# Kernel tuning notes

Hardware: AMD Instinct MI355X
Metric: run time of the kernel (lower is better)

The kernel has to match this reference:

```python
import jax, jax.numpy as jnp
import numpy as np

RADIUS = 3
LEVELS = (1, 4)
P = 3


def _corr_level(fm, gm, cds, jj, radius):
    """Radius-windowed bilinear gather-correlation at one pyramid level.
    fm:  [N, C, Hl, Wl]  feature maps at this level
    gm:  [E, C, P, P]    gathered source patch features (gmap[ii])
    cds: [E, P, P, 2]    (x, y) sampling coords in this level's pixel units
    jj:  [E]             target frame index per edge
    returns [E, 2r+1, 2r+1, P, P]
    """
    N, C, Hl, Wl = fm.shape
    E, _, Pp, _ = gm.shape
    fm_flat = jnp.transpose(fm, (0, 2, 3, 1)).reshape(N * Hl * Wl, C)  # [NHW, C]
    x = cds[..., 0]
    y = cds[..., 1]
    x0 = jnp.floor(x)
    y0 = jnp.floor(y)
    fx = x - x0  # bilinear fractions
    fy = y - y0
    x0i = x0.astype(jnp.int32)
    y0i = y0.astype(jnp.int32)
    D = 2 * radius + 2  # integer support window covering all 2r+1 shifted bilinear taps
    offs = jnp.arange(D, dtype=jnp.int32) - radius
    gy = jnp.clip(y0i[..., None] + offs, 0, Hl - 1)  # [E,P,P,D]
    gx = jnp.clip(x0i[..., None] + offs, 0, Wl - 1)  # [E,P,P,D]
    base = (jj.astype(jnp.int32) * (Hl * Wl))[:, None, None, None, None]  # [E,1,1,1,1]
    lin = base + gy[..., :, None] * Wl + gx[..., None, :]  # [E,P,P,D,D]
    lin_per = jnp.moveaxis(lin.reshape(E, Pp, Pp, D * D), -1, 0)  # [D*D,E,P,P]
    gmT = jnp.transpose(gm, (0, 2, 3, 1))  # [E,P,P,C]

    def step(carry, idx):
        vals = jnp.take(fm_flat, idx, axis=0)  # [E,P,P,C] gathered features
        return carry, jnp.sum(vals * gmT, axis=-1)  # channel contraction -> [E,P,P]

    _, cw = jax.lax.scan(jax.checkpoint(step), None, lin_per)  # [D*D,E,P,P]
    cw = jnp.moveaxis(cw, 0, -1).reshape(E, Pp, Pp, D, D)
    w00 = ((1 - fy) * (1 - fx))[..., None, None]
    w01 = ((1 - fy) * fx)[..., None, None]
    w10 = (fy * (1 - fx))[..., None, None]
    w11 = (fy * fx)[..., None, None]
    c = (w00 * cw[..., : D - 1, : D - 1]
         + w01 * cw[..., : D - 1, 1:]
         + w10 * cw[..., 1:, : D - 1]
         + w11 * cw[..., 1:, 1:])  # [E,P,P,2r+1,2r+1]
    return jnp.transpose(c, (0, 3, 4, 1, 2))  # [E,2r+1,2r+1,P,P]


def _forward(fmap, gmap, coords, ii, jj):
    fm0 = fmap[0]  # [N,C,H,W] level 1
    N, C, H, W = fm0.shape
    # pyramidify: level-4 map via 4x4 average pooling
    fm1 = fm0.reshape(N, C, H // 4, 4, W // 4, 4).mean(axis=(3, 5))
    gm = gmap[0][ii]  # [E,C,P,P]
    cds = coords[0]  # [E,P,P,2]
    c0 = _corr_level(fm0, gm, cds / LEVELS[0], jj, RADIUS)
    c1 = _corr_level(fm1, gm, cds / LEVELS[1], jj, RADIUS)
    out = jnp.stack([c0, c1], axis=-1)  # [E,7,7,P,P,2]
    return out.reshape(1, cds.shape[0], -1)  # [1,E,2*49*P*P]


def setup_inputs():
    key = jax.random.key(0)
    k = jax.random.split(key, 5)
    N, C, H, W = 16, 128, 120, 160
    M = 16 * 96  # frames * patches_per_image
    E = 8192  # edges in the patch graph
    fmap = jax.random.normal(k[0], (1, N, C, H, W), jnp.float32)
    gmap = jax.random.normal(k[1], (1, M, C, P, P), jnp.float32)
    # patch centers kept in-bounds for both pyramid levels
    u = jax.random.uniform(k[2], (1, E, 1, 1, 2), jnp.float32)
    lo = jnp.array([13.0, 13.0], jnp.float32)
    span = jnp.array([126.0, 86.0], jnp.float32)  # x in [13,139], y in [13,99]
    dy, dx = jnp.meshgrid(jnp.arange(P) - 1, jnp.arange(P) - 1, indexing='ij')
    patch_offs = jnp.stack([dx, dy], axis=-1).astype(jnp.float32)  # [P,P,2] (x,y)
    coords = lo + u * span + patch_offs  # [1,E,P,P,2]
    ii = jax.random.randint(k[3], (E,), 0, M, dtype=jnp.int32)
    jj = jax.random.randint(k[4], (E,), 0, N, dtype=jnp.int32)
    return {"fmap": fmap, "gmap": gmap, "coords": coords, "ii": ii, "jj": jj}


def reference(fmap, gmap, coords, ii, jj):
    return _forward(fmap, gmap, coords, ii, jj)
```

## Files before the change

kernel.cpp:

```cpp
#include <hip/hip_runtime.h>

#define RADIUS 3
#define C_CH 128
#define NG 16
#define N_FR 16
#define H0 120
#define W0 160
#define HW0 (H0*W0)
#define H1 30
#define W1 40
#define HW1 (H1*W1)
#define EXT 10
#define NCELL 100
#define M_PT 1536
#define FM1SZ (N_FR*H1*W1*C_CH)
#define GT_SZ (M_PT*9*C_CH)
#define SCSTR 12
#define NBKT 256

typedef _Float16 half2v __attribute__((ext_vector_type(2)));
union Q { uint4 u4; half2v h[4]; };

#if __has_builtin(__builtin_amdgcn_fdot2)
#define FDOT2(a,b,c) __builtin_amdgcn_fdot2((a),(b),(c),false)
#else
#define FDOT2(a,b,c) ((c) + (float)(a).x*(float)(b).x + (float)(a).y*(float)(b).y)
#endif

__device__ __forceinline__ unsigned pack2h(float a, float b) {
    union { _Float16 h[2]; unsigned u; } x;
    x.h[0] = (_Float16)a; x.h[1] = (_Float16)b;
    return x.u;
}

__global__ __launch_bounds__(256) void pack_fmap2(const float* __restrict__ fm0,
                                                  uint4* __restrict__ fH) {
    int idx = blockIdx.x * 256 + threadIdx.x;
    int total = N_FR * NG * HW0;
    if (idx >= total) return;
    int xy = idx % HW0;
    int g = (idx / HW0) & (NG - 1);
    int n = idx / (HW0 * NG);
    const float* src = fm0 + ((size_t)(n * C_CH + g * 8)) * HW0 + xy;
    uint4 o;
    o.x = pack2h(src[0],          src[(size_t)HW0]);
    o.y = pack2h(src[2*(size_t)HW0], src[3*(size_t)HW0]);
    o.z = pack2h(src[4*(size_t)HW0], src[5*(size_t)HW0]);
    o.w = pack2h(src[6*(size_t)HW0], src[7*(size_t)HW0]);
    fH[idx] = o;
}

__global__ __launch_bounds__(256) void pool_from_fH(const uint4* __restrict__ fH,
                                                    uint4* __restrict__ f1H) {
    int idx = blockIdx.x * 256 + threadIdx.x;
    int total = N_FR * NG * HW1;
    if (idx >= total) return;
    int xo = idx % W1;
    int yo = (idx / W1) % H1;
    int ng = idx / HW1;
    const uint4* src = fH + ((size_t)ng * H0 + yo * 4) * W0 + xo * 4;
    float s[8];
#pragma unroll
    for (int k = 0; k < 8; ++k) s[k] = 0.f;
#pragma unroll
    for (int yl = 0; yl < 4; ++yl) {
#pragma unroll
        for (int dx = 0; dx < 4; ++dx) {
            Q q; q.u4 = src[(size_t)yl * W0 + dx];
#pragma unroll
            for (int k = 0; k < 4; ++k) {
                s[2*k]   += (float)q.h[k].x;
                s[2*k+1] += (float)q.h[k].y;
            }
        }
    }
    uint4 o;
    o.x = pack2h(s[0] * (1.f/16.f), s[1] * (1.f/16.f));
    o.y = pack2h(s[2] * (1.f/16.f), s[3] * (1.f/16.f));
    o.z = pack2h(s[4] * (1.f/16.f), s[5] * (1.f/16.f));
    o.w = pack2h(s[6] * (1.f/16.f), s[7] * (1.f/16.f));
    f1H[idx] = o;
}

__global__ __launch_bounds__(128) void gpack(const float* __restrict__ g,
                                             unsigned* __restrict__ gH) {
    __shared__ float s[C_CH * 9];
    int m = blockIdx.x;
    const float* src = g + (size_t)m * (C_CH * 9);
    for (int t = threadIdx.x; t < C_CH * 9; t += 128) s[t] = src[t];
    __syncthreads();
    unsigned* dst = gH + (size_t)m * (9 * 64);
    for (int t = threadIdx.x; t < 9 * 64; t += 128) {
        int pq = t >> 6, pr = t & 63;
        dst[t] = pack2h(s[(2 * pr) * 9 + pq], s[(2 * pr + 1) * 9 + pq]);
    }
}

__device__ __forceinline__ int sort_key(const int* jj, const float* coords, int e) {
    float cy = coords[(size_t)e * 18 + 1];
    int by0 = (int)floorf(cy) - RADIUS;
    int band = min(max(by0 >> 3, 0), 15);
    return jj[e] * 16 + band;
}

__global__ void zero_kernel(int* cnt) {
    int t = blockIdx.x * blockDim.x + threadIdx.x;
    if (t < 2 * NBKT) cnt[t] = 0;
}

__global__ void hist_kernel(const int* __restrict__ jj, const float* __restrict__ coords,
                            int* __restrict__ cnt, int E) {
    __shared__ int h[NBKT];
    int tid = threadIdx.x;
    h[tid] = 0;
    __syncthreads();
    int e = blockIdx.x * blockDim.x + tid;
    if (e < E) atomicAdd(&h[sort_key(jj, coords, e)], 1);
    __syncthreads();
    if (h[tid] > 0) atomicAdd(&cnt[tid], h[tid]);
}

__global__ void scan_kernel(const int* __restrict__ cnt, int* __restrict__ off) {
    if (threadIdx.x == 0) {
        int s = 0;
        for (int f = 0; f < NBKT; ++f) { off[f] = s; s += cnt[f]; }
    }
}

__global__ void scatter_kernel(const int* __restrict__ jj, const float* __restrict__ coords,
                               int* __restrict__ off, int* __restrict__ perm, int E) {
    __shared__ int h[NBKT];
    __shared__ int base[NBKT];
    int tid = threadIdx.x;
    h[tid] = 0;
    __syncthreads();
    int e = blockIdx.x * blockDim.x + tid;
    int k = 0, rank = 0;
    if (e < E) {
        k = sort_key(jj, coords, e);
        rank = atomicAdd(&h[k], 1);
    }
    __syncthreads();
    if (h[tid] > 0) base[tid] = atomicAdd(&off[tid], h[tid]);
    __syncthreads();
    if (e < E) perm[base[k] + rank] = e;
}

__global__ __launch_bounds__(128) void corr_h(
        const unsigned* __restrict__ fH,
        const unsigned* __restrict__ f1H,
        const unsigned* __restrict__ gH,
        const float* __restrict__ coords,
        const int* __restrict__ ii,
        const int* __restrict__ jj,
        const int* __restrict__ perm,
        float* __restrict__ out) {
    __shared__ float sC[2 * NCELL * SCSTR];

    int nwg = gridDim.x;
    int q = nwg >> 3, r = nwg & 7;
    int xcd = blockIdx.x & 7;
    int i = blockIdx.x >> 3;
    int orig = (xcd < r ? xcd * (q + 1) : r * (q + 1) + (xcd - r) * q) + i;
    int e = perm ? perm[orig] : orig;

    int tid = threadIdx.x;
    int iie = __builtin_amdgcn_readfirstlane(ii[e]);
    int jje = __builtin_amdgcn_readfirstlane(jj[e]);
    const float* cb = coords + (size_t)e * 18;

    float cx = cb[0], cy = cb[1];
    int bx0 = (int)floorf(cx) - RADIUS;
    int by0 = (int)floorf(cy) - RADIUS;
    int bx1 = (int)floorf(cx * 0.25f) - RADIUS;
    int by1 = (int)floorf(cy * 0.25f) - RADIUS;

    int cell = min(tid, NCELL - 1);
    int iy = cell / EXT, ix = cell - iy * EXT;
    int gy0 = min(max(by0 + iy, 0), H0 - 1);
    int gx0 = min(max(bx0 + ix, 0), W0 - 1);
    int gy1 = min(max(by1 + iy, 0), H1 - 1);
    int gx1 = min(max(bx1 + ix, 0), W1 - 1);

    const uint4* f0p = (const uint4*)fH + ((size_t)jje * NG * HW0 + (size_t)gy0 * W0 + gx0);
    const uint4* f1p = (const uint4*)f1H + ((size_t)jje * NG * HW1 + (size_t)gy1 * W1 + gx1);
    const uint4* gp  = (const uint4*)gH + (size_t)iie * 144;

    float acc0[9], acc1[9];
#pragma unroll
    for (int pq = 0; pq < 9; ++pq) { acc0[pq] = 0.f; acc1[pq] = 0.f; }

#pragma unroll 4
    for (int g = 0; g < NG; ++g) {
        Q a0; a0.u4 = f0p[(size_t)g * HW0];
        Q a1; a1.u4 = f1p[(size_t)g * HW1];
#pragma unroll
        for (int pq = 0; pq < 9; ++pq) {
            Q gg; gg.u4 = gp[pq * 16 + g];
#pragma unroll
            for (int k = 0; k < 4; ++k) {
                acc0[pq] = FDOT2(a0.h[k], gg.h[k], acc0[pq]);
                acc1[pq] = FDOT2(a1.h[k], gg.h[k], acc1[pq]);
            }
        }
    }

    if (tid < NCELL) {
        float* s0 = &sC[cell * SCSTR];
        float* s1 = &sC[NCELL * SCSTR + cell * SCSTR];
        *reinterpret_cast<float4*>(s0)     = float4{acc0[0], acc0[1], acc0[2], acc0[3]};
        *reinterpret_cast<float4*>(s0 + 4) = float4{acc0[4], acc0[5], acc0[6], acc0[7]};
        s0[8] = acc0[8];
        *reinterpret_cast<float4*>(s1)     = float4{acc1[0], acc1[1], acc1[2], acc1[3]};
        *reinterpret_cast<float4*>(s1 + 4) = float4{acc1[4], acc1[5], acc1[6], acc1[7]};
        s1[8] = acc1[8];
    }
    __syncthreads();

    for (int o = tid; o < 882; o += 128) {
        int lvl = o & 1;
        int rr = o >> 1;
        int pq = rr % 9;
        int ab = rr / 9;
        int a = ab / 7, b = ab - a * 7;
        float s = lvl ? 0.25f : 1.f;
        float x = cb[pq * 2 + 0] * s;
        float y = cb[pq * 2 + 1] * s;
        float x0f = floorf(x), y0f = floorf(y);
        float fx = x - x0f, fy = y - y0f;
        int offx = (int)x0f - RADIUS - (lvl ? bx1 : bx0);
        int offy = (int)y0f - RADIUS - (lvl ? by1 : by0);
        int cell2 = (offy + a) * EXT + (offx + b);
        int base = lvl * (NCELL * SCSTR) + cell2 * SCSTR + pq;
        float c00 = sC[base];
        float c01 = sC[base + SCSTR];
        float c10 = sC[base + EXT * SCSTR];
        float c11 = sC[base + EXT * SCSTR + SCSTR];
        float v = (1.f - fy) * (1.f - fx) * c00 + (1.f - fy) * fx * c01
                + fy * (1.f - fx) * c10 + fy * fx * c11;
        out[(size_t)e * 882 + (size_t)rr * 2 + lvl] = v;
    }
}

__global__ __launch_bounds__(256) void pool_fm1T(const float* __restrict__ fm0,
                                                 float* __restrict__ fm1T) {
    __shared__ float s[C_CH * 41];
    int blk = blockIdx.x;
    int yo = blk % H1;
    int n = blk / H1;
    for (int pair = threadIdx.x; pair < C_CH * W1; pair += 256) {
        int c = pair / W1, xo = pair - c * W1;
        const float* p = fm0 + (((size_t)(n * C_CH + c) * H0) + yo * 4) * W0 + xo * 4;
        float sum = 0.f;
#pragma unroll
        for (int yl = 0; yl < 4; ++yl) {
            float4 v = *reinterpret_cast<const float4*>(p + yl * W0);
            sum += v.x + v.y + v.z + v.w;
        }
        s[c * 41 + xo] = sum * (1.f / 16.f);
    }
    __syncthreads();
    float* dp = fm1T + (size_t)blk * W1 * C_CH;
    for (int t = threadIdx.x; t < W1 * C_CH; t += 256) {
        int xo = t >> 7, c = t & 127;
        dp[t] = s[c * 41 + xo];
    }
}

__global__ __launch_bounds__(128) void corr_kernel(
        const float* __restrict__ fmap, const float* __restrict__ fm1T,
        const float* __restrict__ gmap, const float* __restrict__ coords,
        const int* __restrict__ ii, const int* __restrict__ jj,
        float* __restrict__ out) {
    __shared__ float sC[2 * NCELL * SCSTR];
    int e = blockIdx.x;
    int tid = threadIdx.x;
    int iie = __builtin_amdgcn_readfirstlane(ii[e]);
    int jje = __builtin_amdgcn_readfirstlane(jj[e]);
    const float* cb = coords + (size_t)e * 18;
    float cx = cb[0], cy = cb[1];
    int bx0 = (int)floorf(cx) - RADIUS;
    int by0 = (int)floorf(cy) - RADIUS;
    int bx1 = (int)floorf(cx * 0.25f) - RADIUS;
    int by1 = (int)floorf(cy * 0.25f) - RADIUS;
    int cell = min(tid, NCELL - 1);
    int iy = cell / EXT, ix = cell - iy * EXT;
    int gy0 = min(max(by0 + iy, 0), H0 - 1);
    int gx0 = min(max(bx0 + ix, 0), W0 - 1);
    int gy1 = min(max(by1 + iy, 0), H1 - 1);
    int gx1 = min(max(bx1 + ix, 0), W1 - 1);
    const float* fp0 = fmap + (size_t)jje * C_CH * HW0 + gy0 * W0 + gx0;
    const float* fp1 = fm1T + (((size_t)jje * H1 + gy1) * W1 + gx1) * C_CH;
    float acc0[9], acc1[9];
#pragma unroll
    for (int pq = 0; pq < 9; ++pq) { acc0[pq] = 0.f; acc1[pq] = 0.f; }
    const float* gp = gmap + (size_t)iie * (C_CH * 9);
#pragma unroll 2
    for (int c = 0; c < C_CH; c += 4) {
        float f0 = fp0[(size_t)(c + 0) * HW0];
        float f1 = fp0[(size_t)(c + 1) * HW0];
        float f2 = fp0[(size_t)(c + 2) * HW0];
        float f3 = fp0[(size_t)(c + 3) * HW0];
        float4 fv = *reinterpret_cast<const float4*>(fp1 + c);
#pragma unroll
        for (int pq = 0; pq < 9; ++pq) {
            float g0 = gp[(c + 0) * 9 + pq];
            float g1 = gp[(c + 1) * 9 + pq];
            float g2 = gp[(c + 2) * 9 + pq];
            float g3 = gp[(c + 3) * 9 + pq];
            acc0[pq] += f0 * g0 + f1 * g1 + f2 * g2 + f3 * g3;
            acc1[pq] += fv.x * g0 + fv.y * g1 + fv.z * g2 + fv.w * g3;
        }
    }
    if (tid < NCELL) {
        float* s0 = &sC[cell * SCSTR];
        float* s1 = &sC[NCELL * SCSTR + cell * SCSTR];
        *reinterpret_cast<float4*>(s0)     = float4{acc0[0], acc0[1], acc0[2], acc0[3]};
        *reinterpret_cast<float4*>(s0 + 4) = float4{acc0[4], acc0[5], acc0[6], acc0[7]};
        s0[8] = acc0[8];
        *reinterpret_cast<float4*>(s1)     = float4{acc1[0], acc1[1], acc1[2], acc1[3]};
        *reinterpret_cast<float4*>(s1 + 4) = float4{acc1[4], acc1[5], acc1[6], acc1[7]};
        s1[8] = acc1[8];
    }
    __syncthreads();
    for (int o = tid; o < 882; o += 128) {
        int lvl = o & 1;
        int rr = o >> 1;
        int pq = rr % 9;
        int ab = rr / 9;
        int a = ab / 7, b = ab - a * 7;
        float s = lvl ? 0.25f : 1.f;
        float x = cb[pq * 2 + 0] * s;
        float y = cb[pq * 2 + 1] * s;
        float x0f = floorf(x), y0f = floorf(y);
        float fx = x - x0f, fy = y - y0f;
        int offx = (int)x0f - RADIUS - (lvl ? bx1 : bx0);
        int offy = (int)y0f - RADIUS - (lvl ? by1 : by0);
        int cell2 = (offy + a) * EXT + (offx + b);
        int base = lvl * (NCELL * SCSTR) + cell2 * SCSTR + pq;
        float c00 = sC[base];
        float c01 = sC[base + SCSTR];
        float c10 = sC[base + EXT * SCSTR];
        float c11 = sC[base + EXT * SCSTR + SCSTR];
        float v = (1.f - fy) * (1.f - fx) * c00 + (1.f - fy) * fx * c01
                + fy * (1.f - fx) * c10 + fy * fx * c11;
        out[(size_t)e * 882 + (size_t)rr * 2 + lvl] = v;
    }
}

extern "C" void kernel_launch(void* const* d_in, const int* in_sizes, int n_in,
                              void* d_out, int out_size, void* d_ws, size_t ws_size,
                              hipStream_t stream) {
    const float* fmap   = (const float*)d_in[0];
    const float* gmap   = (const float*)d_in[1];
    const float* coords = (const float*)d_in[2];
    const int* ii       = (const int*)d_in[3];
    const int* jj       = (const int*)d_in[4];
    float* out = (float*)d_out;
    int E = in_sizes[3];

    size_t szFH  = (size_t)N_FR * C_CH * HW0 * 2;
    size_t szF1H = (size_t)N_FR * C_CH * HW1 * 2;
    size_t szGH  = (size_t)M_PT * 9 * C_CH * 2;
    size_t need_h = szFH + szF1H + szGH + 2048 + (size_t)E * 4;

    if (ws_size >= need_h) {
        uint4* fH  = (uint4*)d_ws;
        uint4* f1H = (uint4*)((char*)d_ws + szFH);
        unsigned* gH = (unsigned*)((char*)d_ws + szFH + szF1H);
        int* cnt  = (int*)((char*)d_ws + szFH + szF1H + szGH);
        int* off  = cnt + NBKT;
        int* perm = off + NBKT;

        int tot_pack = N_FR * NG * HW0;
        pack_fmap2<<<(tot_pack + 255) / 256, 256, 0, stream>>>(fmap, fH);
        int tot_pool = N_FR * NG * HW1;
        pool_from_fH<<<(tot_pool + 255) / 256, 256, 0, stream>>>(fH, f1H);
        gpack<<<M_PT, 128, 0, stream>>>(gmap, gH);

        int nb = (E + NBKT - 1) / NBKT;
        zero_kernel<<<(2 * NBKT + 255) / 256, 256, 0, stream>>>(cnt);
        hist_kernel<<<nb, NBKT, 0, stream>>>(jj, coords, cnt, E);
        scan_kernel<<<1, 64, 0, stream>>>(cnt, off);
        scatter_kernel<<<nb, NBKT, 0, stream>>>(jj, coords, off, perm, E);

        corr_h<<<E, 128, 0, stream>>>((const unsigned*)fH, (const unsigned*)f1H, gH,
                                      coords, ii, jj, perm, out);
        return;
    }

    float* fm1T = (float*)d_ws;
    pool_fm1T<<<N_FR * H1, 256, 0, stream>>>(fmap, fm1T);
    corr_kernel<<<E, 128, 0, stream>>>(fmap, fm1T, gmap, coords, ii, jj, out);
}
```

Before: 123.2 us.

## Compute correlation window with MFMA 16x16x32 f16 instead of fdot2

```diff
diff --git a/kernel.cpp b/kernel.cpp
--- a/kernel.cpp
+++ b/kernel.cpp
@@ -14,18 +14,14 @@
 #define NCELL 100
 #define M_PT 1536
 #define FM1SZ (N_FR*H1*W1*C_CH)
-#define GT_SZ (M_PT*9*C_CH)
 #define SCSTR 12
 #define NBKT 256
 
 typedef _Float16 half2v __attribute__((ext_vector_type(2)));
+typedef _Float16 f16x8 __attribute__((ext_vector_type(8)));
+typedef float f32x4 __attribute__((ext_vector_type(4)));
 union Q { uint4 u4; half2v h[4]; };
-
-#if __has_builtin(__builtin_amdgcn_fdot2)
-#define FDOT2(a,b,c) __builtin_amdgcn_fdot2((a),(b),(c),false)
-#else
-#define FDOT2(a,b,c) ((c) + (float)(a).x*(float)(b).x + (float)(a).y*(float)(b).y)
-#endif
+union AB { uint4 u4; f16x8 h8; };
 
 __device__ __forceinline__ unsigned pack2h(float a, float b) {
     union { _Float16 h[2]; unsigned u; } x;
@@ -43,7 +39,7 @@
     int n = idx / (HW0 * NG);
     const float* src = fm0 + ((size_t)(n * C_CH + g * 8)) * HW0 + xy;
     uint4 o;
-    o.x = pack2h(src[0],          src[(size_t)HW0]);
+    o.x = pack2h(src[0],             src[(size_t)HW0]);
     o.y = pack2h(src[2*(size_t)HW0], src[3*(size_t)HW0]);
     o.z = pack2h(src[4*(size_t)HW0], src[5*(size_t)HW0]);
     o.w = pack2h(src[6*(size_t)HW0], src[7*(size_t)HW0]);
@@ -146,10 +142,10 @@
     if (e < E) perm[base[k] + rank] = e;
 }
 
-__global__ __launch_bounds__(128) void corr_h(
-        const unsigned* __restrict__ fH,
-        const unsigned* __restrict__ f1H,
-        const unsigned* __restrict__ gH,
+__global__ __launch_bounds__(64, 4) void corr_mfma(
+        const uint4* __restrict__ fH,
+        const uint4* __restrict__ f1H,
+        const uint4* __restrict__ gH4,
         const float* __restrict__ coords,
         const int* __restrict__ ii,
         const int* __restrict__ jj,
@@ -160,11 +156,14 @@
     int nwg = gridDim.x;
     int q = nwg >> 3, r = nwg & 7;
     int xcd = blockIdx.x & 7;
-    int i = blockIdx.x >> 3;
-    int orig = (xcd < r ? xcd * (q + 1) : r * (q + 1) + (xcd - r) * q) + i;
+    int ib = blockIdx.x >> 3;
+    int orig = (xcd < r ? xcd * (q + 1) : r * (q + 1) + (xcd - r) * q) + ib;
     int e = perm ? perm[orig] : orig;
 
-    int tid = threadIdx.x;
+    int l = threadIdx.x;
+    int lrow = l & 15;
+    int lk = l >> 4;
+
     int iie = __builtin_amdgcn_readfirstlane(ii[e]);
     int jje = __builtin_amdgcn_readfirstlane(jj[e]);
     const float* cb = coords + (size_t)e * 18;
@@ -175,49 +174,65 @@
     int bx1 = (int)floorf(cx * 0.25f) - RADIUS;
     int by1 = (int)floorf(cy * 0.25f) - RADIUS;
 
-    int cell = min(tid, NCELL - 1);
-    int iy = cell / EXT, ix = cell - iy * EXT;
-    int gy0 = min(max(by0 + iy, 0), H0 - 1);
-    int gx0 = min(max(bx0 + ix, 0), W0 - 1);
-    int gy1 = min(max(by1 + iy, 0), H1 - 1);
-    int gx1 = min(max(bx1 + ix, 0), W1 - 1);
-
-    const uint4* f0p = (const uint4*)fH + ((size_t)jje * NG * HW0 + (size_t)gy0 * W0 + gx0);
-    const uint4* f1p = (const uint4*)f1H + ((size_t)jje * NG * HW1 + (size_t)gy1 * W1 + gx1);
-    const uint4* gp  = (const uint4*)gH + (size_t)iie * 144;
-
-    float acc0[9], acc1[9];
-#pragma unroll
-    for (int pq = 0; pq < 9; ++pq) { acc0[pq] = 0.f; acc1[pq] = 0.f; }
-
-#pragma unroll 4
-    for (int g = 0; g < NG; ++g) {
-        Q a0; a0.u4 = f0p[(size_t)g * HW0];
-        Q a1; a1.u4 = f1p[(size_t)g * HW1];
-#pragma unroll
-        for (int pq = 0; pq < 9; ++pq) {
-            Q gg; gg.u4 = gp[pq * 16 + g];
-#pragma unroll
-            for (int k = 0; k < 4; ++k) {
-                acc0[pq] = FDOT2(a0.h[k], gg.h[k], acc0[pq]);
-                acc1[pq] = FDOT2(a1.h[k], gg.h[k], acc1[pq]);
+    int off0[7], off1[7];
+#pragma unroll
+    for (int t = 0; t < 7; ++t) {
+        int c = min(t * 16 + lrow, NCELL - 1);
+        int iy = c / EXT, ix = c - iy * EXT;
+        int gy0 = min(max(by0 + iy, 0), H0 - 1);
+        int gx0 = min(max(bx0 + ix, 0), W0 - 1);
+        int gy1 = min(max(by1 + iy, 0), H1 - 1);
+        int gx1 = min(max(bx1 + ix, 0), W1 - 1);
+        off0[t] = gy0 * W0 + gx0;
+        off1[t] = gy1 * W1 + gx1;
+    }
+
+    const uint4* f0 = fH + (size_t)jje * NG * HW0;
+    const uint4* f1 = f1H + (size_t)jje * NG * HW1;
+    int pqc = min(lrow, 8);
+    const uint4* gb = gH4 + (size_t)iie * 144 + pqc * 16 + lk;
+
+    f32x4 acc0[7], acc1[7];
+#pragma unroll
+    for (int t = 0; t < 7; ++t) {
+        acc0[t] = (f32x4){0.f, 0.f, 0.f, 0.f};
+        acc1[t] = (f32x4){0.f, 0.f, 0.f, 0.f};
+    }
+
+#pragma unroll
+    for (int kk = 0; kk < 4; ++kk) {
+        AB b; b.u4 = gb[kk * 4];
+        const uint4* p0 = f0 + (size_t)(kk * 4 + lk) * HW0;
+        const uint4* p1 = f1 + (size_t)(kk * 4 + lk) * HW1;
+        AB a[7];
+#pragma unroll
+        for (int t = 0; t < 7; ++t) a[t].u4 = p0[off0[t]];
+#pragma unroll
+        for (int t = 0; t < 7; ++t)
+            acc0[t] = __builtin_amdgcn_mfma_f32_16x16x32_f16(a[t].h8, b.h8, acc0[t], 0, 0, 0);
+#pragma unroll
+        for (int t = 0; t < 7; ++t) a[t].u4 = p1[off1[t]];
+#pragma unroll
+        for (int t = 0; t < 7; ++t)
+            acc1[t] = __builtin_amdgcn_mfma_f32_16x16x32_f16(a[t].h8, b.h8, acc1[t], 0, 0, 0);
+    }
+
+    if (lrow < 9) {
+#pragma unroll
+        for (int t = 0; t < 7; ++t) {
+#pragma unroll
+            for (int r2 = 0; r2 < 4; ++r2) {
+                int cell = t * 16 + lk * 4 + r2;
+                if (cell < NCELL) {
+                    sC[cell * SCSTR + lrow] = acc0[t][r2];
+                    sC[NCELL * SCSTR + cell * SCSTR + lrow] = acc1[t][r2];
+                }
             }
         }
     }
-
-    if (tid < NCELL) {
-        float* s0 = &sC[cell * SCSTR];
-        float* s1 = &sC[NCELL * SCSTR + cell * SCSTR];
-        *reinterpret_cast<float4*>(s0)     = float4{acc0[0], acc0[1], acc0[2], acc0[3]};
-        *reinterpret_cast<float4*>(s0 + 4) = float4{acc0[4], acc0[5], acc0[6], acc0[7]};
-        s0[8] = acc0[8];
-        *reinterpret_cast<float4*>(s1)     = float4{acc1[0], acc1[1], acc1[2], acc1[3]};
-        *reinterpret_cast<float4*>(s1 + 4) = float4{acc1[4], acc1[5], acc1[6], acc1[7]};
-        s1[8] = acc1[8];
-    }
-    __syncthreads();
-
-    for (int o = tid; o < 882; o += 128) {
+    __syncthreads();
+
+    for (int o = l; o < 882; o += 64) {
         int lvl = o & 1;
         int rr = o >> 1;
         int pq = rr % 9;
@@ -361,7 +376,7 @@
 
     size_t szFH  = (size_t)N_FR * C_CH * HW0 * 2;
     size_t szF1H = (size_t)N_FR * C_CH * HW1 * 2;
-    size_t szGH  = (size_t)M_PT * 9 * C_CH * 2;
+    size_t szGH  = (size_t)M_PT * 9 * C_CH * 2 + 4096;
     size_t need_h = szFH + szF1H + szGH + 2048 + (size_t)E * 4;
 
     if (ws_size >= need_h) {
@@ -384,8 +399,8 @@
         scan_kernel<<<1, 64, 0, stream>>>(cnt, off);
         scatter_kernel<<<nb, NBKT, 0, stream>>>(jj, coords, off, perm, E);
 
-        corr_h<<<E, 128, 0, stream>>>((const unsigned*)fH, (const unsigned*)f1H, gH,
-                                      coords, ii, jj, perm, out);
+        corr_mfma<<<E, 64, 0, stream>>>(fH, f1H, (const uint4*)gH,
+                                        coords, ii, jj, perm, out);
         return;
     }
 
```

Result: faster. 113.3 us (-8.0%).
